# Performance work log

Hardware: AMD Instinct MI355X
Metric: run time of the kernel (lower is better)

Reference implementation:

```python
import jax, jax.numpy as jnp
import numpy as np

N, M, K = 4096, 256, 32
W_EPS = 1e-6


def _spd(key, n, k):
    # well-conditioned SPD precision matrices: A A^T / k + I
    a = jax.random.normal(key, (n, k, k), dtype=jnp.float32)
    return jnp.matmul(a, jnp.swapaxes(a, -1, -2)) / k + jnp.eye(k, dtype=jnp.float32)


def setup_inputs() -> dict:
    key = jax.random.key(0)
    k1, k2, k3, k4 = jax.random.split(key, 4)
    W = jax.random.uniform(k1, (N, M), dtype=jnp.float32)
    mu_s = jax.random.normal(k2, (N, K), dtype=jnp.float32)
    omega_child = _spd(k3, N, K)
    omega_parent = _spd(k4, M, K)
    return {"W": W, "mu_s": mu_s, "omega_child": omega_child, "omega_parent": omega_parent}


def reference(W, mu_s, omega_child, omega_parent):
    # mask out negligible memberships (original skips w < 1e-6)
    wT = W.T                                   # (M, N)
    mask = wT >= W_EPS
    w = jnp.where(mask, wT, 0.0)

    # v_i = inv(omega_child_i) @ mu_s_i  -> batched solve, (N, K)
    v = jnp.linalg.solve(omega_child, mu_s[..., None])[..., 0]

    # transported means: Omega_alpha @ v_i, (M, N, K)
    T = jnp.einsum('mkl,nl->mnk', omega_parent, v)

    Z = w.sum(-1)                              # (M,)
    Zs = jnp.maximum(Z, 1e-30)
    mu_bar = jnp.einsum('mn,mnk->mk', w, T) / Zs[:, None]
    diff = T - mu_bar[:, None, :]              # (M, N, K)
    var = jnp.einsum('mn,mnk->mk', w, diff * diff) / Zs[:, None]
    psi = var.sum(-1)                          # (M,)

    # clusters with fewer than 2 contributing agents get psi = 0
    count = mask.sum(-1)
    return jnp.where(count >= 2, psi, 0.0)
```

## Files before the change

### kernel.cpp

```cpp
#include <hip/hip_runtime.h>

constexpr int N_AG = 4096;
constexpr int M_CL = 256;
constexpr int KD   = 32;
constexpr float WEPS = 1e-6f;

constexpr int PART_STRIDE = 1088;
constexpr int V_OFF  = M_CL * 4 * PART_STRIDE;
constexpr int VT_OFF = V_OFF + N_AG * KD;
constexpr int WT_OFF = VT_OFF + N_AG * KD;

typedef __attribute__((ext_vector_type(8))) short short8;
typedef __attribute__((ext_vector_type(4))) float f32x4;

__device__ __forceinline__ float rlane(float x, int l) {
    return __int_as_float(__builtin_amdgcn_readlane(__float_as_int(x), l));
}

template<int J>
struct GJ {
    static __device__ __forceinline__ void run(float (&col)[32]) {
        const float piv  = rlane(col[J], J);
        const float pinv = 1.0f / piv;
        col[J] *= pinv;
        #pragma unroll
        for (int i = 0; i < 32; ++i) {
            if (i == J) continue;
            const float fi = rlane(col[i], J);
            col[i] = fmaf(-fi, col[J], col[i]);
        }
        GJ<J + 1>::run(col);
    }
};
template<> struct GJ<32> {
    static __device__ __forceinline__ void run(float (&)[32]) {}
};

__global__ __launch_bounds__(256, 1) void solve_kernel(const float* __restrict__ oc,
                                                       const float* __restrict__ mu,
                                                       float* __restrict__ v) {
    const int lane = threadIdx.x & 63;
    const int wid  = threadIdx.x >> 6;
    const int idx  = blockIdx.x * 4 + wid;
    const int c = (lane < 32) ? lane : 32;

    float col[32];
    #pragma unroll
    for (int i = 0; i < 32; ++i) {
        col[i] = (c < 32) ? oc[idx * 1024 + i * 32 + c]
                          : mu[idx * 32 + i];
    }

    GJ<0>::run(col);

    float res = 0.0f;
    #pragma unroll
    for (int i = 0; i < 32; ++i) {
        const float xi = rlane(col[i], 32);
        if (lane == i) res = xi;
    }
    if (lane < 32) v[idx * 32 + lane] = res;
}

__global__ __launch_bounds__(256) void transpose_fused(const float* __restrict__ W,
                                                       const float* __restrict__ v,
                                                       float* __restrict__ Wt,
                                                       float* __restrict__ vT) {
    __shared__ float tb[32][33];
    const int x = threadIdx.x & 31;
    const int y = threadIdx.x >> 5;
    const int bid = blockIdx.x;
    if (bid < 1024) {
        const int n0 = (bid & 127) * 32;
        const int m0 = (bid >> 7) * 32;
        #pragma unroll
        for (int r = 0; r < 4; ++r) {
            const int n = y + 8 * r;
            float w = W[(size_t)(n0 + n) * 256 + m0 + x];
            tb[n][x] = (w >= WEPS) ? w : 0.0f;
        }
        __syncthreads();
        #pragma unroll
        for (int r = 0; r < 4; ++r) {
            const int mm = y + 8 * r;
            Wt[(size_t)(m0 + mm) * 4096 + n0 + x] = tb[x][mm];
        }
    } else {
        const int n0 = (bid - 1024) * 32;
        #pragma unroll
        for (int r = 0; r < 4; ++r) {
            const int n = y + 8 * r;
            tb[n][x] = v[(size_t)(n0 + n) * 32 + x];
        }
        __syncthreads();
        #pragma unroll
        for (int r = 0; r < 4; ++r) {
            const int kk = y + 8 * r;
            vT[(size_t)kk * 4096 + n0 + x] = tb[x][kk];
        }
    }
}

__global__ __launch_bounds__(256, 3) void partial_kernel(const float* __restrict__ Wt,
                                                         const float* __restrict__ vT,
                                                         float* __restrict__ wsout) {
    const int m = blockIdx.x >> 2;
    const int p = blockIdx.x & 3;
    const int t = threadIdx.x;
    const int lane = t & 63;
    const int wv   = t >> 6;

    __shared__ unsigned ubuf[4][2][32 * 36];
    __shared__ float swbuf[1024];
    __shared__ float zred[256];
    __shared__ float s1buf[32];

    const float4 wv4 = reinterpret_cast<const float4*>(Wt + (size_t)m * 4096 + p * 1024)[t];
    float zacc = wv4.x + wv4.y + wv4.z + wv4.w;
    float cacc = (wv4.x >= WEPS ? 1.f : 0.f) + (wv4.y >= WEPS ? 1.f : 0.f)
               + (wv4.z >= WEPS ? 1.f : 0.f) + (wv4.w >= WEPS ? 1.f : 0.f);
    reinterpret_cast<float4*>(swbuf)[t] =
        make_float4(sqrtf(wv4.x), sqrtf(wv4.y), sqrtf(wv4.z), sqrtf(wv4.w));
    if (t < 32) s1buf[t] = 0.0f;
    __syncthreads();

    f32x4 Chh[4], Chl[4];
    #pragma unroll
    for (int q = 0; q < 4; ++q) {
        Chh[q] = (f32x4){0.f, 0.f, 0.f, 0.f};
        Chl[q] = (f32x4){0.f, 0.f, 0.f, 0.f};
    }
    float s1acc[4] = {0.f, 0.f, 0.f, 0.f};

    const int krow = lane >> 3;
    const int nsub = (lane & 7) * 4;

    for (int rnd = 0; rnd < 4; ++rnd) {
        const int nloc0 = wv * 256 + rnd * 64;

        #pragma unroll
        for (int it = 0; it < 8; ++it) {
            const int k  = krow + 8 * (it & 3);
            const int nn = nsub + 32 * (it >> 2);
            const float4 v4 = *reinterpret_cast<const float4*>(
                vT + (size_t)k * 4096 + p * 1024 + nloc0 + nn);
            const float4 s4 = *reinterpret_cast<const float4*>(&swbuf[nloc0 + nn]);
            const float ux = v4.x * s4.x, uy = v4.y * s4.y;
            const float uz = v4.z * s4.z, uw = v4.w * s4.w;
            const unsigned bx = __float_as_uint(ux), by = __float_as_uint(uy);
            const unsigned bz = __float_as_uint(uz), bw = __float_as_uint(uw);
            const unsigned hi01 = __builtin_amdgcn_perm(by, bx, 0x07060302u);
            const unsigned hi23 = __builtin_amdgcn_perm(bw, bz, 0x07060302u);
            const float lx = ux - __uint_as_float(bx & 0xFFFF0000u);
            const float ly = uy - __uint_as_float(by & 0xFFFF0000u);
            const float lz = uz - __uint_as_float(bz & 0xFFFF0000u);
            const float lw = uw - __uint_as_float(bw & 0xFFFF0000u);
            const unsigned lo01 = __builtin_amdgcn_perm(__float_as_uint(ly), __float_as_uint(lx), 0x07060302u);
            const unsigned lo23 = __builtin_amdgcn_perm(__float_as_uint(lw), __float_as_uint(lz), 0x07060302u);
            const int dwi = k * 36 + (nn >> 1);
            *reinterpret_cast<uint2*>(&ubuf[wv][0][dwi]) = make_uint2(hi01, hi23);
            *reinterpret_cast<uint2*>(&ubuf[wv][1][dwi]) = make_uint2(lo01, lo23);
            s1acc[it & 3] += ux * s4.x + uy * s4.y + uz * s4.z + uw * s4.w;
        }

        #pragma unroll
        for (int c2 = 0; c2 < 2; ++c2) {
            const int ndw = (c2 * 32 + (lane >> 4) * 8) >> 1;
            const int r0 = (lane & 15) * 36 + ndw;
            const int r1 = r0 + 16 * 36;
            const short8 h0 = *reinterpret_cast<const short8*>(&ubuf[wv][0][r0]);
            const short8 h1 = *reinterpret_cast<const short8*>(&ubuf[wv][0][r1]);
            const short8 l0 = *reinterpret_cast<const short8*>(&ubuf[wv][1][r0]);
            const short8 l1 = *reinterpret_cast<const short8*>(&ubuf[wv][1][r1]);
            Chh[0] = __builtin_amdgcn_mfma_f32_16x16x32_bf16(h0, h0, Chh[0], 0, 0, 0);
            Chh[1] = __builtin_amdgcn_mfma_f32_16x16x32_bf16(h0, h1, Chh[1], 0, 0, 0);
            Chh[2] = __builtin_amdgcn_mfma_f32_16x16x32_bf16(h1, h0, Chh[2], 0, 0, 0);
            Chh[3] = __builtin_amdgcn_mfma_f32_16x16x32_bf16(h1, h1, Chh[3], 0, 0, 0);
            Chl[0] = __builtin_amdgcn_mfma_f32_16x16x32_bf16(h0, l0, Chl[0], 0, 0, 0);
            Chl[1] = __builtin_amdgcn_mfma_f32_16x16x32_bf16(h0, l1, Chl[1], 0, 0, 0);
            Chl[2] = __builtin_amdgcn_mfma_f32_16x16x32_bf16(h1, l0, Chl[2], 0, 0, 0);
            Chl[3] = __builtin_amdgcn_mfma_f32_16x16x32_bf16(h1, l1, Chl[3], 0, 0, 0);
        }
    }

    #pragma unroll
    for (int j = 0; j < 4; ++j) {
        float r = s1acc[j];
        r += __shfl_xor(r, 1);
        r += __shfl_xor(r, 2);
        r += __shfl_xor(r, 4);
        if ((lane & 7) == 0) atomicAdd(&s1buf[krow + 8 * j], r);
    }
    __syncthreads();

    float* redw = reinterpret_cast<float*>(&ubuf[wv][0][0]);
    #pragma unroll
    for (int q = 0; q < 4; ++q) {
        const int I = q >> 1, J = q & 1;
        #pragma unroll
        for (int r = 0; r < 4; ++r) {
            const int a = I * 16 + (lane >> 4) * 4 + r;
            const int b = J * 16 + (lane & 15);
            redw[a * 32 + b] = Chh[q][r] + Chl[q][r];
        }
    }
    __syncthreads();
    #pragma unroll
    for (int q = 0; q < 4; ++q) {
        const int I = q >> 1, J = q & 1;
        #pragma unroll
        for (int r = 0; r < 4; ++r) {
            const int a = I * 16 + (lane >> 4) * 4 + r;
            const int b = J * 16 + (lane & 15);
            redw[b * 32 + a] += Chl[q][r];
        }
    }
    __syncthreads();

    const size_t base = (size_t)(m * 4 + p) * PART_STRIDE;
    float o0 = 0.f, o1 = 0.f, o2 = 0.f, o3 = 0.f;
    #pragma unroll
    for (int ww = 0; ww < 4; ++ww) {
        const float4 x = *reinterpret_cast<const float4*>(
            &reinterpret_cast<float*>(&ubuf[ww][0][0])[t * 4]);
        o0 += x.x; o1 += x.y; o2 += x.z; o3 += x.w;
    }
    *reinterpret_cast<float4*>(&wsout[base + t * 4]) = make_float4(o0, o1, o2, o3);

    zred[t] = zacc; __syncthreads();
    #pragma unroll
    for (int s = 128; s > 0; s >>= 1) {
        if (t < s) zred[t] += zred[t + s];
        __syncthreads();
    }
    if (t == 0) wsout[base + 1056] = zred[0];
    __syncthreads();
    zred[t] = cacc; __syncthreads();
    #pragma unroll
    for (int s = 128; s > 0; s >>= 1) {
        if (t < s) zred[t] += zred[t + s];
        __syncthreads();
    }
    if (t == 0) wsout[base + 1057] = zred[0];
    if (t < 32) wsout[base + 1024 + t] = s1buf[t];
}

__global__ __launch_bounds__(256) void combine_kernel(const float* __restrict__ op,
                                                      const float* __restrict__ ws,
                                                      float* __restrict__ out) {
    const int m = blockIdx.x;
    const int t = threadIdx.x;

    __shared__ float omg[32 * 33];
    __shared__ float vbar[32];
    __shared__ float red[256];

    #pragma unroll
    for (int i = 0; i < 4; ++i) {
        const int g = t + 256 * i;
        const int r = g >> 5, cc = g & 31;
        omg[r * 33 + cc] = op[(size_t)m * 1024 + g];
    }

    const size_t mb = (size_t)m * 4 * PART_STRIDE;
    float Z = 0.0f, cnt = 0.0f, s1 = 0.0f;
    float s2[4] = {0.f, 0.f, 0.f, 0.f};
    #pragma unroll
    for (int p2 = 0; p2 < 4; ++p2) {
        const size_t bp = mb + (size_t)p2 * PART_STRIDE;
        Z   += ws[bp + 1056];
        cnt += ws[bp + 1057];
        if (t < 32) s1 += ws[bp + 1024 + t];
        const float4 sp = *reinterpret_cast<const float4*>(&ws[bp + t * 4]);
        s2[0] += sp.x; s2[1] += sp.y; s2[2] += sp.z; s2[3] += sp.w;
    }
    const float invZ = 1.0f / fmaxf(Z, 1e-30f);
    if (t < 32) vbar[t] = s1 * invZ;
    __syncthreads();

    const int k  = t >> 3;
    const int l0 = (t & 7) * 4;
    float G[4] = {0.f, 0.f, 0.f, 0.f};
    #pragma unroll
    for (int i = 0; i < 32; ++i) {
        const float ok = omg[i * 33 + k];
        #pragma unroll
        for (int q = 0; q < 4; ++q) G[q] = fmaf(ok, omg[i * 33 + l0 + q], G[q]);
    }

    const float vk = vbar[k];
    float val = 0.0f;
    #pragma unroll
    for (int q = 0; q < 4; ++q)
        val += G[q] * (s2[q] * invZ - vk * vbar[l0 + q]);

    red[t] = val; __syncthreads();
    #pragma unroll
    for (int s = 128; s > 0; s >>= 1) {
        if (t < s) red[t] += red[t + s];
        __syncthreads();
    }
    if (t == 0) out[m] = (cnt >= 1.5f) ? red[0] : 0.0f;
}

extern "C" void kernel_launch(void* const* d_in, const int* in_sizes, int n_in,
                              void* d_out, int out_size, void* d_ws, size_t ws_size,
                              hipStream_t stream) {
    const float* W  = (const float*)d_in[0];
    const float* mu = (const float*)d_in[1];
    const float* oc = (const float*)d_in[2];
    const float* op = (const float*)d_in[3];
    float* out = (float*)d_out;
    float* ws  = (float*)d_ws;

    solve_kernel<<<1024, 256, 0, stream>>>(oc, mu, ws + V_OFF);
    transpose_fused<<<1152, 256, 0, stream>>>(W, ws + V_OFF, ws + WT_OFF, ws + VT_OFF);
    partial_kernel<<<1024, 256, 0, stream>>>(ws + WT_OFF, ws + VT_OFF, ws);
    combine_kernel<<<256, 256, 0, stream>>>(op, ws, out);
}
```

Baseline: 115.2 us.

## Fuse solve into transpose kernel and combine into partial via last-block atomic

The batched Gauss-Jordan solve now runs inside the same launch as the W transpose, and each solve block writes its four v vectors straight into the transposed vT layout, so the separate v buffer and its transpose pass go away. The combine step is folded into partial_kernel: each cluster's fourth finishing block, detected with a per-cluster atomic counter and thread fences, does the final reduction. This cuts four launches to two and removes launch gaps and one intermediate round trip. In exchange it adds fence and atomic overhead, the vT writes are narrow and scattered, and the counters must be zeroed in prep_kernel on every call.

```diff
diff --git a/kernel.cpp b/kernel.cpp
--- a/kernel.cpp
+++ b/kernel.cpp
@@ -6,9 +6,10 @@
 constexpr float WEPS = 1e-6f;
 
 constexpr int PART_STRIDE = 1088;
-constexpr int V_OFF  = M_CL * 4 * PART_STRIDE;
-constexpr int VT_OFF = V_OFF + N_AG * KD;
-constexpr int WT_OFF = VT_OFF + N_AG * KD;
+constexpr int PART_SZ = M_CL * 4 * PART_STRIDE;
+constexpr int VT_OFF  = PART_SZ;
+constexpr int WT_OFF  = VT_OFF + N_AG * KD;
+constexpr int CNT_OFF = WT_OFF + N_AG * M_CL;
 
 typedef __attribute__((ext_vector_type(8))) short short8;
 typedef __attribute__((ext_vector_type(4))) float f32x4;
@@ -36,43 +37,21 @@
     static __device__ __forceinline__ void run(float (&)[32]) {}
 };
 
-__global__ __launch_bounds__(256, 1) void solve_kernel(const float* __restrict__ oc,
-                                                       const float* __restrict__ mu,
-                                                       float* __restrict__ v) {
-    const int lane = threadIdx.x & 63;
-    const int wid  = threadIdx.x >> 6;
-    const int idx  = blockIdx.x * 4 + wid;
-    const int c = (lane < 32) ? lane : 32;
-
-    float col[32];
-    #pragma unroll
-    for (int i = 0; i < 32; ++i) {
-        col[i] = (c < 32) ? oc[idx * 1024 + i * 32 + c]
-                          : mu[idx * 32 + i];
-    }
-
-    GJ<0>::run(col);
-
-    float res = 0.0f;
-    #pragma unroll
-    for (int i = 0; i < 32; ++i) {
-        const float xi = rlane(col[i], 32);
-        if (lane == i) res = xi;
-    }
-    if (lane < 32) v[idx * 32 + lane] = res;
-}
-
-__global__ __launch_bounds__(256) void transpose_fused(const float* __restrict__ W,
-                                                       const float* __restrict__ v,
-                                                       float* __restrict__ Wt,
-                                                       float* __restrict__ vT) {
+__global__ __launch_bounds__(256) void prep_kernel(const float* __restrict__ W,
+                                                   const float* __restrict__ mu,
+                                                   const float* __restrict__ oc,
+                                                   float* __restrict__ ws) {
     __shared__ float tb[32][33];
-    const int x = threadIdx.x & 31;
-    const int y = threadIdx.x >> 5;
+    __shared__ float sv[4][32];
     const int bid = blockIdx.x;
+    const int t   = threadIdx.x;
+
     if (bid < 1024) {
+        const int x = t & 31;
+        const int y = t >> 5;
         const int n0 = (bid & 127) * 32;
         const int m0 = (bid >> 7) * 32;
+        float* Wt = ws + WT_OFF;
         #pragma unroll
         for (int r = 0; r < 4; ++r) {
             const int n = y + 8 * r;
@@ -86,24 +65,45 @@
             Wt[(size_t)(m0 + mm) * 4096 + n0 + x] = tb[x][mm];
         }
     } else {
-        const int n0 = (bid - 1024) * 32;
-        #pragma unroll
-        for (int r = 0; r < 4; ++r) {
-            const int n = y + 8 * r;
-            tb[n][x] = v[(size_t)(n0 + n) * 32 + x];
-        }
-        __syncthreads();
-        #pragma unroll
-        for (int r = 0; r < 4; ++r) {
-            const int kk = y + 8 * r;
-            vT[(size_t)kk * 4096 + n0 + x] = tb[x][kk];
+        if (bid == 1024) {
+            reinterpret_cast<unsigned*>(ws + CNT_OFF)[t & 255] = 0u;
+        }
+        const int lane = t & 63;
+        const int wid  = t >> 6;
+        const int n0   = (bid - 1024) * 4;
+        const int idx  = n0 + wid;
+        const int c = (lane < 32) ? lane : 32;
+
+        float col[32];
+        #pragma unroll
+        for (int i = 0; i < 32; ++i) {
+            col[i] = (c < 32) ? oc[(size_t)idx * 1024 + i * 32 + c]
+                              : mu[(size_t)idx * 32 + i];
+        }
+        GJ<0>::run(col);
+
+        float res = 0.0f;
+        #pragma unroll
+        for (int i = 0; i < 32; ++i) {
+            const float xi = rlane(col[i], 32);
+            if (lane == i) res = xi;
+        }
+        if (lane < 32) sv[wid][lane] = res;
+        __syncthreads();
+        if (t < 128) {
+            const int k = t >> 2;
+            const int j = t & 3;
+            ws[VT_OFF + (size_t)k * 4096 + n0 + j] = sv[j][k];
         }
     }
 }
 
 __global__ __launch_bounds__(256, 3) void partial_kernel(const float* __restrict__ Wt,
                                                          const float* __restrict__ vT,
-                                                         float* __restrict__ wsout) {
+                                                         float* __restrict__ wsout,
+                                                         const float* __restrict__ op,
+                                                         unsigned* __restrict__ cnt,
+                                                         float* __restrict__ out) {
     const int m = blockIdx.x >> 2;
     const int p = blockIdx.x & 3;
     const int t = threadIdx.x;
@@ -114,6 +114,7 @@
     __shared__ float swbuf[1024];
     __shared__ float zred[256];
     __shared__ float s1buf[32];
+    __shared__ unsigned lastf;
 
     const float4 wv4 = reinterpret_cast<const float4*>(Wt + (size_t)m * 4096 + p * 1024)[t];
     float zacc = wv4.x + wv4.y + wv4.z + wv4.w;
@@ -243,39 +244,35 @@
     }
     if (t == 0) wsout[base + 1057] = zred[0];
     if (t < 32) wsout[base + 1024 + t] = s1buf[t];
-}
-
-__global__ __launch_bounds__(256) void combine_kernel(const float* __restrict__ op,
-                                                      const float* __restrict__ ws,
-                                                      float* __restrict__ out) {
-    const int m = blockIdx.x;
-    const int t = threadIdx.x;
-
-    __shared__ float omg[32 * 33];
-    __shared__ float vbar[32];
-    __shared__ float red[256];
-
+
+    __syncthreads();
+    __threadfence();
+    if (t == 0) lastf = atomicAdd(cnt + m, 1u);
+    __syncthreads();
+    if (lastf != 3u) return;
+    __threadfence();
+
+    float* omg = reinterpret_cast<float*>(&ubuf[0][0][0]);
     #pragma unroll
     for (int i = 0; i < 4; ++i) {
         const int g = t + 256 * i;
-        const int r = g >> 5, cc = g & 31;
-        omg[r * 33 + cc] = op[(size_t)m * 1024 + g];
-    }
-
+        omg[(g >> 5) * 33 + (g & 31)] = op[(size_t)m * 1024 + g];
+    }
     const size_t mb = (size_t)m * 4 * PART_STRIDE;
-    float Z = 0.0f, cnt = 0.0f, s1 = 0.0f;
+    float Zt = 0.0f, ct = 0.0f, s1 = 0.0f;
     float s2[4] = {0.f, 0.f, 0.f, 0.f};
     #pragma unroll
     for (int p2 = 0; p2 < 4; ++p2) {
         const size_t bp = mb + (size_t)p2 * PART_STRIDE;
-        Z   += ws[bp + 1056];
-        cnt += ws[bp + 1057];
-        if (t < 32) s1 += ws[bp + 1024 + t];
-        const float4 sp = *reinterpret_cast<const float4*>(&ws[bp + t * 4]);
+        Zt += wsout[bp + 1056];
+        ct += wsout[bp + 1057];
+        if (t < 32) s1 += wsout[bp + 1024 + t];
+        const float4 sp = *reinterpret_cast<const float4*>(&wsout[bp + t * 4]);
         s2[0] += sp.x; s2[1] += sp.y; s2[2] += sp.z; s2[3] += sp.w;
     }
-    const float invZ = 1.0f / fmaxf(Z, 1e-30f);
-    if (t < 32) vbar[t] = s1 * invZ;
+    const float invZ = 1.0f / fmaxf(Zt, 1e-30f);
+    __syncthreads();
+    if (t < 32) s1buf[t] = s1 * invZ;
     __syncthreads();
 
     const int k  = t >> 3;
@@ -287,20 +284,19 @@
         #pragma unroll
         for (int q = 0; q < 4; ++q) G[q] = fmaf(ok, omg[i * 33 + l0 + q], G[q]);
     }
-
-    const float vk = vbar[k];
+    const float vk = s1buf[k];
     float val = 0.0f;
     #pragma unroll
     for (int q = 0; q < 4; ++q)
-        val += G[q] * (s2[q] * invZ - vk * vbar[l0 + q]);
-
-    red[t] = val; __syncthreads();
+        val += G[q] * (s2[q] * invZ - vk * s1buf[l0 + q]);
+
+    zred[t] = val; __syncthreads();
     #pragma unroll
     for (int s = 128; s > 0; s >>= 1) {
-        if (t < s) red[t] += red[t + s];
-        __syncthreads();
-    }
-    if (t == 0) out[m] = (cnt >= 1.5f) ? red[0] : 0.0f;
+        if (t < s) zred[t] += zred[t + s];
+        __syncthreads();
+    }
+    if (t == 0) out[m] = (ct >= 1.5f) ? zred[0] : 0.0f;
 }
 
 extern "C" void kernel_launch(void* const* d_in, const int* in_sizes, int n_in,
@@ -313,8 +309,7 @@
     float* out = (float*)d_out;
     float* ws  = (float*)d_ws;
 
-    solve_kernel<<<1024, 256, 0, stream>>>(oc, mu, ws + V_OFF);
-    transpose_fused<<<1152, 256, 0, stream>>>(W, ws + V_OFF, ws + WT_OFF, ws + VT_OFF);
-    partial_kernel<<<1024, 256, 0, stream>>>(ws + WT_OFF, ws + VT_OFF, ws);
-    combine_kernel<<<256, 256, 0, stream>>>(op, ws, out);
+    prep_kernel<<<2048, 256, 0, stream>>>(W, mu, oc, ws);
+    partial_kernel<<<1024, 256, 0, stream>>>(ws + WT_OFF, ws + VT_OFF, ws,
+                                             op, (unsigned*)(ws + CNT_OFF), out);
 }
```

Result: slower. 235.0 us (+104.0%).
